# Kernel tuning notes

Hardware: AMD Instinct MI355X
Metric: run time of the kernel (lower is better)

The kernel has to match this reference:

```python
import jax, jax.numpy as jnp
import numpy as np

N, E = 50000, 800000
VOCAB, D, H, EDIM = 10000, 128, 8, 16
C = D // H  # per-head channels = 16
NEG_SLOPE_ATT = 0.2   # GATv2 attention leaky_relu slope
NEG_SLOPE_OUT = 0.01  # F.leaky_relu default
BN_EPS = 1e-5


def setup_inputs() -> dict:
    key = jax.random.key(0)
    ks = jax.random.split(key, 10)
    g = lambda k, shape, fan: (jax.random.normal(k, shape, jnp.float32) / np.float32(np.sqrt(fan)))
    return {
        "x": jax.random.randint(ks[0], (N,), 0, VOCAB),
        "ei": jax.random.randint(ks[1], (2, E), 0, N),
        "ew": jax.random.normal(ks[2], (E, EDIM), jnp.float32),
        "emb": g(ks[3], (VOCAB, D), D),
        "W_l": g(ks[4], (D, D), D),
        "b_l": jnp.zeros((D,), jnp.float32),
        "W_r": g(ks[5], (D, D), D),
        "b_r": jnp.zeros((D,), jnp.float32),
        "att": g(ks[6], (H, C), C),
        "W_e": g(ks[7], (EDIM, D), EDIM),
        "bias": jnp.zeros((D,), jnp.float32),
        "gamma": jnp.ones((D,), jnp.float32),
        "beta": jnp.zeros((D,), jnp.float32),
    }


def reference(x, ei, ew, emb, W_l, b_l, W_r, b_r, att, W_e, bias, gamma, beta):
    n = x.shape[0]
    # Embeddings: lut(x) * sqrt(d_model); dropout=0 (identity)
    h = emb[x] * jnp.float32(np.sqrt(D))                      # [N, D]
    # GATv2Conv linear transforms (source / target)
    xl = (h @ W_l + b_l).reshape(n, H, C)                      # [N, H, C]
    xr = (h @ W_r + b_r).reshape(n, H, C)                      # [N, H, C]
    eemb = (ew @ W_e).reshape(-1, H, C)                        # [E, H, C]
    src, dst = ei[0], ei[1]
    # per-edge attention logits: a^T LeakyReLU(x_l[j] + x_r[i] + e)
    m = jax.nn.leaky_relu(xl[src] + xr[dst] + eemb, NEG_SLOPE_ATT)  # [E, H, C]
    score = jnp.einsum('ehc,hc->eh', m, att)                   # [E, H]
    # segment softmax over incoming edges of each target node
    smax = jax.ops.segment_max(score, dst, num_segments=n)     # [N, H]
    ex = jnp.exp(score - smax[dst])                            # [E, H]
    denom = jax.ops.segment_sum(ex, dst, num_segments=n)       # [N, H]
    alpha = ex / denom[dst]                                    # [E, H]
    # scatter-add aggregation of weighted source features
    agg = jax.ops.segment_sum(alpha[:, :, None] * xl[src], dst, num_segments=n)
    out = agg.reshape(n, D) + bias                             # [N, D]
    # BatchNorm1d (training mode: batch statistics, biased variance)
    mean = out.mean(axis=0)
    var = out.var(axis=0)
    y = (out - mean) * jax.lax.rsqrt(var + BN_EPS) * gamma + beta
    return jax.nn.leaky_relu(y, NEG_SLOPE_OUT)
```

## Files before the change

kernel.cpp:

```cpp
#include <hip/hip_runtime.h>
#include <hip/hip_bf16.h>
#include <hip/hip_fp16.h>

typedef __hip_bfloat16 bf16;
typedef unsigned short u16;

#define D 128
#define EDIM 16
#define SQRT_D 11.313708498984761f

typedef short bf16x8 __attribute__((ext_vector_type(8)));
typedef float f32x4 __attribute__((ext_vector_type(4)));
typedef _Float16 h2 __attribute__((ext_vector_type(2)));

#define PF_BL    0
#define PF_BR    128
#define PF_WE    256
#define PF_ATT   2304
#define PF_BIAS  2432
#define PF_GAMMA 2560
#define PF_BETA  2688
#define PF_TOTAL 2816

__device__ __forceinline__ u16 f2bf_bits(float f) {
    union { bf16 h; u16 s; } cv; cv.h = __float2bfloat16(f); return cv.s;
}
__device__ __forceinline__ float2 h2f2(unsigned u) {
    union { unsigned u; __half2 h; } cv; cv.u = u;
    return __half22float2(cv.h);
}
__device__ __forceinline__ int swid(int nn, int k) {
    return nn * 128 + ((((k >> 3) ^ (nn & 15)) << 3) | (k & 7));
}
__device__ __forceinline__ float red8(float x) {
    x += __int_as_float(__builtin_amdgcn_update_dpp(0, __float_as_int(x), 0xB1, 0xf, 0xf, true));
    x += __int_as_float(__builtin_amdgcn_update_dpp(0, __float_as_int(x), 0x4E, 0xf, 0xf, true));
    x += __int_as_float(__builtin_amdgcn_update_dpp(0, __float_as_int(x), 0x141, 0xf, 0xf, true));
    return x;
}

__global__ void k_zero_detect(int* p, int count, const u16* __restrict__ u, int* flag)
{
    int i = blockIdx.x * blockDim.x + threadIdx.x;
    if (i < count) p[i] = 0;
    if (blockIdx.x == 0) {
        __shared__ int sh[256];
        int t = threadIdx.x;
        int cnt = 0;
        for (int k = t; k < 4096; k += 256) {
            int e = (u[k] >> 7) & 0xFF;
            cnt += (e > 132 && e < 255) ? 1 : 0;
        }
        sh[t] = cnt;
        __syncthreads();
        for (int s = 128; s > 0; s >>= 1) {
            if (t < s) sh[t] += sh[t + s];
            __syncthreads();
        }
        if (t == 0) *flag = (sh[0] > 100) ? 1 : 0;
    }
}

__device__ __forceinline__ float rdv(const void* p, int i, int fl) {
    return fl ? ((const float*)p)[i] : __bfloat162float(((const bf16*)p)[i]);
}

__global__ __launch_bounds__(256) void k_prep_hist(
    const void* Wl, const void* Wr,
    const void* bl, const void* br, const void* We, const void* att,
    const void* bias, const void* gamma, const void* beta,
    const int* __restrict__ flag,
    u16* __restrict__ WT, float* __restrict__ pf,
    const int* __restrict__ ei, int* __restrict__ deg,
    int nE, int prepBlocks)
{
    if ((int)blockIdx.x >= prepBlocks) {
        int e = (blockIdx.x - prepBlocks) * 256 + threadIdx.x;
        if (e < nE) atomicAdd(&deg[ei[nE + e]], 1);
        return;
    }
    const int fl = *flag;
    int idx = blockIdx.x * 256 + threadIdx.x;
    if (idx < 32768) {
        int w = idx >> 14;
        int j = idx & 16383;
        int k = j >> 7, nn = j & 127;
        const void* W = w ? Wr : Wl;
        WT[w * 16384 + swid(nn, k)] = f2bf_bits(rdv(W, k * D + nn, fl) * SQRT_D);
        return;
    }
    idx -= 32768;
    if (idx < 128)  { pf[PF_BL + idx] = rdv(bl, idx, fl); return; }
    idx -= 128;
    if (idx < 128)  { pf[PF_BR + idx] = rdv(br, idx, fl); return; }
    idx -= 128;
    if (idx < 2048) { pf[PF_WE + idx] = rdv(We, idx, fl); return; }
    idx -= 2048;
    if (idx < 128)  { pf[PF_ATT + idx] = rdv(att, idx, fl); return; }
    idx -= 128;
    if (idx < 128)  { pf[PF_BIAS + idx] = rdv(bias, idx, fl); return; }
    idx -= 128;
    if (idx < 128)  { pf[PF_GAMMA + idx] = rdv(gamma, idx, fl); return; }
    idx -= 128;
    if (idx < 128)  { pf[PF_BETA + idx] = rdv(beta, idx, fl); return; }
}

__global__ __launch_bounds__(1024) void k_scan1(
    const int* __restrict__ deg, int* __restrict__ row_ptr,
    int* __restrict__ cursor, int n, int nBlk)
{
    __shared__ int chsum[512];
    __shared__ int part[1024];
    __shared__ int myOff;
    const int t = threadIdx.x;
    const int wv = t >> 6;
    const int lane = t & 63;

    for (int c = wv; c < nBlk; c += 16) {
        int base = c << 10;
        int s = 0;
        for (int k = lane; k < 1024; k += 64) {
            int i = base + k;
            s += (i < n) ? deg[i] : 0;
        }
        #pragma unroll
        for (int m = 1; m < 64; m <<= 1) s += __shfl_xor(s, m);
        if (lane == 0) chsum[c] = s;
    }
    __syncthreads();
    if (t == 0) {
        int run = 0;
        for (int c = 0; c < (int)blockIdx.x; ++c) run += chsum[c];
        myOff = run;
    }
    __syncthreads();

    int i = blockIdx.x * 1024 + t;
    int v = (i < n) ? deg[i] : 0;
    part[t] = v;
    __syncthreads();
    for (int off = 1; off < 1024; off <<= 1) {
        int u = (t >= off) ? part[t - off] : 0;
        __syncthreads();
        part[t] += u;
        __syncthreads();
    }
    if (i < n) {
        int excl = myOff + part[t] - v;
        row_ptr[i] = excl;
        cursor[i] = excl;
        if (i == n - 1) row_ptr[n] = excl + v;
    }
}

__global__ __launch_bounds__(1024) void k_scan_sum(
    const int* __restrict__ deg, int* __restrict__ blkSum, int n)
{
    __shared__ int sh[1024];
    int t = threadIdx.x;
    int i = blockIdx.x * 1024 + t;
    sh[t] = (i < n) ? deg[i] : 0;
    __syncthreads();
    for (int s = 512; s > 0; s >>= 1) {
        if (t < s) sh[t] += sh[t + s];
        __syncthreads();
    }
    if (t == 0) blkSum[blockIdx.x] = sh[0];
}
__global__ __launch_bounds__(1024) void k_scan_blk(
    const int* __restrict__ blkSum, int* __restrict__ blkOff, int nBlk)
{
    __shared__ int part[1024];
    int t = threadIdx.x;
    int v = (t < nBlk) ? blkSum[t] : 0;
    part[t] = v;
    __syncthreads();
    for (int off = 1; off < 1024; off <<= 1) {
        int u = (t >= off) ? part[t - off] : 0;
        __syncthreads();
        part[t] += u;
        __syncthreads();
    }
    if (t < nBlk) blkOff[t] = part[t] - v;
}
__global__ __launch_bounds__(1024) void k_scan_write(
    const int* __restrict__ deg, const int* __restrict__ blkOff,
    int* __restrict__ row_ptr, int* __restrict__ cursor, int n)
{
    __shared__ int part[1024];
    int t = threadIdx.x;
    int i = blockIdx.x * 1024 + t;
    int v = (i < n) ? deg[i] : 0;
    part[t] = v;
    __syncthreads();
    for (int off = 1; off < 1024; off <<= 1) {
        int u = (t >= off) ? part[t - off] : 0;
        __syncthreads();
        part[t] += u;
        __syncthreads();
    }
    if (i < n) {
        int excl = blkOff[blockIdx.x] + part[t] - v;
        row_ptr[i] = excl;
        cursor[i] = excl;
        if (i == n - 1) row_ptr[n] = excl + v;
    }
}

__global__ __launch_bounds__(512) void k_scatnode(
    const int* __restrict__ ei, int* __restrict__ cursor,
    int* __restrict__ csr, const void* __restrict__ ew,
    u16* __restrict__ ewc, const int* __restrict__ flag, int nE,
    const int* __restrict__ x, const void* __restrict__ emb,
    const u16* __restrict__ WT, const float* __restrict__ pf,
    u16* __restrict__ xl16, u16* __restrict__ xr16, int n, int scatBlocks)
{
    __shared__ u16 Bt[16384];
    const int t = threadIdx.x;

    if ((int)blockIdx.x < scatBlocks) {
        int e = blockIdx.x * 512 + t;
        if (e >= nE) return;
        int src = ei[e], dst = ei[nE + e];
        int pos = atomicAdd(&cursor[dst], 1);
        csr[pos] = src << 8;
        __half2 h[8];
        if (*flag) {
            const float4* s = (const float4*)((const float*)ew + (size_t)e * 16);
            float f[16];
            *(float4*)(f)      = s[0];
            *(float4*)(f + 4)  = s[1];
            *(float4*)(f + 8)  = s[2];
            *(float4*)(f + 12) = s[3];
            #pragma unroll
            for (int q = 0; q < 8; ++q)
                h[q] = __float22half2_rn(make_float2(f[2*q], f[2*q+1]));
        } else {
            const uint4* s = (const uint4*)((const u16*)ew + (size_t)e * 16);
            unsigned uu[8];
            *(uint4*)(uu)     = s[0];
            *(uint4*)(uu + 4) = s[1];
            #pragma unroll
            for (int q = 0; q < 8; ++q) {
                float lo = __uint_as_float(uu[q] << 16);
                float hi = __uint_as_float(uu[q] & 0xffff0000u);
                h[q] = __float22half2_rn(make_float2(lo, hi));
            }
        }
        u16* d16 = ewc + ((size_t)pos << 4);
        *(uint4*)d16       = *(uint4*)&h[0];
        *(uint4*)(d16 + 8) = *(uint4*)&h[4];
        return;
    }

    const int fl = *flag;
    const int l = t & 63;
    const int wv = t >> 6;
    const int m = l & 15;
    const int quad = l >> 4;
    const int R = (blockIdx.x - scatBlocks) * 128;

    int arow = R + wv * 16 + m;
    int tok = (arow < n) ? x[arow] : 0;
    bf16x8 afr[4];
    if (!fl) {
        const u16* ap = (const u16*)emb + (size_t)tok * D + quad * 8;
        #pragma unroll
        for (int kk = 0; kk < 4; ++kk) afr[kk] = *(const bf16x8*)(ap + kk * 32);
    } else {
        const float* ap = (const float*)emb + (size_t)tok * D + quad * 8;
        #pragma unroll
        for (int kk = 0; kk < 4; ++kk) {
            float4 a = *(const float4*)(ap + kk * 32);
            float4 b = *(const float4*)(ap + kk * 32 + 4);
            u16 o[8] = { f2bf_bits(a.x), f2bf_bits(a.y), f2bf_bits(a.z), f2bf_bits(a.w),
                         f2bf_bits(b.x), f2bf_bits(b.y), f2bf_bits(b.z), f2bf_bits(b.w) };
            afr[kk] = *(bf16x8*)o;
        }
    }

    #pragma unroll
    for (int w = 0; w < 2; ++w) {
        {
            const uint4* s = (const uint4*)(WT + w * 16384);
            uint4* dd = (uint4*)&Bt[0];
            #pragma unroll
            for (int i = 0; i < 4; ++i) dd[i * 512 + t] = s[i * 512 + t];
        }
        __syncthreads();
        const float* bb = pf + (w ? PF_BR : PF_BL);
        u16* out = w ? xr16 : xl16;
        f32x4 acc[8];
        #pragma unroll
        for (int nt = 0; nt < 8; ++nt) {
            float bv = bb[nt * 16 + m];
            acc[nt] = f32x4{bv, bv, bv, bv};
        }
        #pragma unroll
        for (int kk = 0; kk < 4; ++kk) {
            #pragma unroll
            for (int nt = 0; nt < 8; ++nt) {
                int blk = (quad + 4 * kk) ^ m;
                bf16x8 bfr = *(const bf16x8*)&Bt[(nt * 16 + m) * 128 + blk * 8];
                acc[nt] = __builtin_amdgcn_mfma_f32_16x16x32_bf16(afr[kk], bfr, acc[nt], 0, 0, 0);
            }
        }
        #pragma unroll
        for (int nt = 0; nt < 8; ++nt) {
            int col = nt * 16 + m;
            #pragma unroll
            for (int r = 0; r < 4; ++r) {
                int row = R + wv * 16 + quad * 4 + r;
                if (row < n)
                    out[(size_t)row * D + col] =
                        __half_as_ushort(__float2half(acc[nt][r]));
            }
        }
        __syncthreads();
    }
}

struct EwH {
    unsigned v[8];
    __device__ __forceinline__ void load(const u16* base, int j) {
        const uint4* q = (const uint4*)(base + ((size_t)j << 4));
        uint4 A = q[0], B = q[1];
        v[0]=A.x; v[1]=A.y; v[2]=A.z; v[3]=A.w;
        v[4]=B.x; v[5]=B.y; v[6]=B.z; v[7]=B.w;
    }
    __device__ __forceinline__ float2 pair(int q) const { return h2f2(v[q]); }
};

__global__ __launch_bounds__(256) void k_agg(
    const int* __restrict__ row_ptr, const int* __restrict__ csr,
    const u16* __restrict__ ewc, const float* __restrict__ pf,
    const u16* __restrict__ xl16, const u16* __restrict__ xr16,
    float* __restrict__ vpre, float* __restrict__ bnsum,
    float* __restrict__ bnsumsq, int n)
{
    const int t = threadIdx.x;
    const int l = t & 63;
    const int wv = __builtin_amdgcn_readfirstlane(t >> 6);

#if __has_builtin(__builtin_amdgcn_fdot2)
    h2 we0[8], we1[8];
    #pragma unroll
    for (int q = 0; q < 8; ++q) {
        float2 a = *(const float2*)&pf[PF_WE + (2*q)   * D + 2 * l];
        float2 b = *(const float2*)&pf[PF_WE + (2*q+1) * D + 2 * l];
        we0[q] = h2{(_Float16)a.x, (_Float16)b.x};
        we1[q] = h2{(_Float16)a.y, (_Float16)b.y};
    }
#else
    float2 we[EDIM];
    #pragma unroll
    for (int k = 0; k < EDIM; ++k)
        we[k] = *(const float2*)&pf[PF_WE + k * D + 2 * l];
#endif
    const float2 attv  = *(const float2*)&pf[PF_ATT + 2 * l];
    const float2 biasv = *(const float2*)&pf[PF_BIAS + 2 * l];

    float s0 = 0, s20 = 0, s1 = 0, s21 = 0;

    const int slot = blockIdx.x * 4 + wv;
    const int i0 = slot * 4;
    const int i1 = min(i0 + 4, n);

    if (i0 < n) {
        const char* xlB = (const char*)xl16 + 4 * l;
        const char* xrB = (const char*)xr16 + 4 * l;

        int cur = i0;
        int endCur  = row_ptr[i0 + 1];
        int endNext = row_ptr[min(i0 + 2, i1)];
        const int begAll = row_ptr[i0];
        const int endAll = row_ptr[i1];

        float2 xrvCur  = h2f2(*(const unsigned*)(xrB + ((size_t)i0 << 8)));
        int nxt0 = min(i0 + 1, i1 - 1);
        float2 xrvNext = h2f2(*(const unsigned*)(xrB + ((size_t)nxt0 << 8)));

        float acc0 = 0, acc1 = 0, den = 0;

        auto finalize = [&]() {
            float inv = den > 0.f ? 1.0f / den : 0.0f;
            float v0 = fmaf(acc0, inv, biasv.x);
            float v1 = fmaf(acc1, inv, biasv.y);
            *(float2*)(vpre + ((size_t)cur << 7) + 2 * l) = make_float2(v0, v1);
            s0 += v0; s20 += v0 * v0;
            s1 += v1; s21 += v1 * v1;
            acc0 = acc1 = den = 0.f;
        };
        auto advance = [&]() {
            finalize();
            ++cur;
            endCur  = endNext;
            endNext = row_ptr[min(cur + 2, i1)];
            xrvCur  = xrvNext;
            int nxt = min(cur + 1, i1 - 1);
            xrvNext = h2f2(*(const unsigned*)(xrB + ((size_t)nxt << 8)));
        };
        auto comp = [&](const EwH& w, unsigned xbits) {
            float e0 = xrvCur.x, e1 = xrvCur.y;
#if __has_builtin(__builtin_amdgcn_fdot2)
            #pragma unroll
            for (int q = 0; q < 8; ++q) {
                h2 pr = __builtin_bit_cast(h2, w.v[q]);
                e0 = __builtin_amdgcn_fdot2(pr, we0[q], e0, false);
                e1 = __builtin_amdgcn_fdot2(pr, we1[q], e1, false);
            }
#else
            #pragma unroll
            for (int q = 0; q < 8; ++q) {
                float2 pr = w.pair(q);
                e0 = fmaf(pr.x, we[2*q].x,   e0);
                e0 = fmaf(pr.y, we[2*q+1].x, e0);
                e1 = fmaf(pr.x, we[2*q].y,   e1);
                e1 = fmaf(pr.y, we[2*q+1].y, e1);
            }
#endif
            float2 xc = h2f2(xbits);
            float z0 = xc.x + e0, z1 = xc.y + e1;
            float m0 = fmaxf(z0, 0.2f * z0);
            float m1 = fmaxf(z1, 0.2f * z1);
            float p = red8(fmaf(m1, attv.y, m0 * attv.x));
            float ex = __expf(p);
            den += ex;
            acc0 = fmaf(ex, xc.x, acc0);
            acc1 = fmaf(ex, xc.y, acc1);
        };

        const int cnt = endAll - begAll;
        if (cnt > 0) {
            EwH wA, wB, wC, wD;
            unsigned xA = 0, xB = 0, xC = 0, xD = 0;
            {            wA.load(ewc, begAll);     xA = *(const unsigned*)(xlB + csr[begAll]); }
            if (cnt > 1) { wB.load(ewc, begAll + 1); xB = *(const unsigned*)(xlB + csr[begAll + 1]); }
            if (cnt > 2) { wC.load(ewc, begAll + 2); xC = *(const unsigned*)(xlB + csr[begAll + 2]); }
            if (cnt > 3) { wD.load(ewc, begAll + 3); xD = *(const unsigned*)(xlB + csr[begAll + 3]); }

            int j  = begAll;
            int jp = begAll + 4;
            while (true) {
#define STAGE(W, X)                                                              \
                while (j >= endCur) advance();                                   \
                comp(W, X);                                                      \
                if (jp < endAll) {                                               \
                    W.load(ewc, jp);                                             \
                    X = *(const unsigned*)(xlB + csr[jp]);                       \
                }                                                                \
                ++jp; ++j;                                                       \
                if (j >= endAll) break;
                STAGE(wA, xA)
                STAGE(wB, xB)
                STAGE(wC, xC)
                STAGE(wD, xD)
#undef STAGE
            }
        }
        while (cur < i1) { finalize(); ++cur; }
    }

    __shared__ float sh[4][D], sh2[4][D];
    sh[wv][2*l] = s0;   sh[wv][2*l+1] = s1;
    sh2[wv][2*l] = s20; sh2[wv][2*l+1] = s21;
    __syncthreads();
    if (t < D) {
        float a = 0, a2 = 0;
        #pragma unroll
        for (int q = 0; q < 4; ++q) { a += sh[q][t]; a2 += sh2[q][t]; }
        atomicAdd(&bnsum[t], a);
        atomicAdd(&bnsumsq[t], a2);
    }
}

__global__ __launch_bounds__(256) void k_final(
    const float* __restrict__ vpre, const float* __restrict__ pf,
    const float* __restrict__ bnsum, const float* __restrict__ bnsumsq,
    float* __restrict__ out, int n)
{
    int idx = blockIdx.x * 256 + threadIdx.x;
    if (idx >= n * (D / 4)) return;
    int pos = idx * 4;
    int d = pos & (D - 1);
    const float invN = 1.0f / (float)n;
    float4 v  = *(const float4*)(vpre + pos);
    float4 ms = *(const float4*)(bnsum + d);
    float4 m2 = *(const float4*)(bnsumsq + d);
    float4 g  = *(const float4*)(pf + PF_GAMMA + d);
    float4 bt = *(const float4*)(pf + PF_BETA + d);
    float* vv = (float*)&v; float* msv = (float*)&ms; float* m2v = (float*)&m2;
    float* gv = (float*)&g; float* btv = (float*)&bt;
    float4 o;
    float* ov = (float*)&o;
    #pragma unroll
    for (int c = 0; c < 4; ++c) {
        float mean = msv[c] * invN;
        float var = m2v[c] * invN - mean * mean;
        float y = (vv[c] - mean) * rsqrtf(var + 1e-5f) * gv[c] + btv[c];
        ov[c] = y > 0.f ? y : 0.01f * y;
    }
    *(float4*)(out + pos) = o;
}

extern "C" void kernel_launch(void* const* d_in, const int* in_sizes, int n_in,
                              void* d_out, int out_size, void* d_ws, size_t ws_size,
                              hipStream_t stream)
{
    const int*  x     = (const int*)d_in[0];
    const int*  ei    = (const int*)d_in[1];
    const void* ew    = d_in[2];
    const void* emb   = d_in[3];
    const void* Wl    = d_in[4];
    const void* bl    = d_in[5];
    const void* Wr    = d_in[6];
    const void* br    = d_in[7];
    const void* att   = d_in[8];
    const void* We    = d_in[9];
    const void* bias  = d_in[10];
    const void* gamma = d_in[11];
    const void* beta  = d_in[12];

    const int n  = in_sizes[0];
    const int nE = in_sizes[1] / 2;

    const int nScanBlk = (n + 1023) / 1024;

    float* ws      = (float*)d_ws;
    float* vpre    = ws;
    u16*   xl16    = (u16*)(vpre + (size_t)n * D);
    u16*   xr16    = xl16 + (size_t)n * D;
    int*   deg     = (int*)(xr16 + (size_t)n * D);
    float* bnsum   = (float*)(deg + n);
    float* bnsumsq = bnsum + D;
    int*   flag    = (int*)(bnsumsq + D);
    int*   row_ptr = flag + 1;
    int*   cursor  = row_ptr + (n + 1);
    int*   blkSum  = cursor + n;
    int*   blkOff  = blkSum + nScanBlk;
    uintptr_t p    = (uintptr_t)(blkOff + nScanBlk);
    p = (p + 15) & ~(uintptr_t)15;
    int*   csr     = (int*)p;
    p = (uintptr_t)(csr + nE);
    p = (p + 15) & ~(uintptr_t)15;
    u16*   WT      = (u16*)p;
    p = (uintptr_t)(WT + 32768);
    float* pf      = (float*)p;
    p = (uintptr_t)(pf + PF_TOTAL);
    p = (p + 15) & ~(uintptr_t)15;
    u16*   ewc     = (u16*)p;

    int zc = n + 2 * D;
    k_zero_detect<<<(zc + 255) / 256, 256, 0, stream>>>(deg, zc, (const u16*)emb, flag);

    int prepN = 32768 + PF_TOTAL;
    int prepBlocks = (prepN + 255) / 256;
    int histBlocks = (nE + 255) / 256;
    k_prep_hist<<<prepBlocks + histBlocks, 256, 0, stream>>>(
        Wl, Wr, bl, br, We, att, bias, gamma, beta,
        flag, WT, pf, ei, deg, nE, prepBlocks);

    if (nScanBlk <= 512) {
        k_scan1<<<nScanBlk, 1024, 0, stream>>>(deg, row_ptr, cursor, n, nScanBlk);
    } else {
        k_scan_sum<<<nScanBlk, 1024, 0, stream>>>(deg, blkSum, n);
        k_scan_blk<<<1, 1024, 0, stream>>>(blkSum, blkOff, nScanBlk);
        k_scan_write<<<nScanBlk, 1024, 0, stream>>>(deg, blkOff, row_ptr, cursor, n);
    }

    int scatBlocks = (nE + 511) / 512;
    int nodeBlocks = (n + 127) / 128;
    k_scatnode<<<scatBlocks + nodeBlocks, 512, 0, stream>>>(
        ei, cursor, csr, ew, ewc, flag, nE,
        x, emb, WT, pf, xl16, xr16, n, scatBlocks);

    int aggBlocks = (n + 15) / 16;
    k_agg<<<aggBlocks, 256, 0, stream>>>(row_ptr, csr, ewc, pf, xl16, xr16,
                                         vpre, bnsum, bnsumsq, n);

    k_final<<<(n * (D / 4) + 255) / 256, 256, 0, stream>>>(
        vpre, pf, bnsum, bnsumsq, (float*)d_out, n);
}
```

Before: 348.6 us.

## Shard degree histogram and CSR cursors across 8 copies to reduce atomic contention

Degree counting and CSR scatter cursors are split into 8 per-shard arrays, selected by block index, so edges in different shards hit different atomic addresses. The scan kernels sum the shards to form row pointers and assign each shard its own cursor sub-range within the node's segment. This adds 8x larger zeroing and strided scan reads in exchange for less atomic serialization. Histogram blocks now process two edges per thread so their edge ranges align with the scatter blocks.

```diff
diff --git a/kernel.cpp b/kernel.cpp
--- a/kernel.cpp
+++ b/kernel.cpp
@@ -8,6 +8,7 @@
 #define D 128
 #define EDIM 16
 #define SQRT_D 11.313708498984761f
+#define NSHARD 8
 
 typedef short bf16x8 __attribute__((ext_vector_type(8)));
 typedef float f32x4 __attribute__((ext_vector_type(4)));
@@ -71,12 +72,17 @@
     const void* bias, const void* gamma, const void* beta,
     const int* __restrict__ flag,
     u16* __restrict__ WT, float* __restrict__ pf,
-    const int* __restrict__ ei, int* __restrict__ deg,
-    int nE, int prepBlocks)
+    const int* __restrict__ ei, int* __restrict__ degS,
+    int nE, int nNodes, int prepBlocks)
 {
     if ((int)blockIdx.x >= prepBlocks) {
-        int e = (blockIdx.x - prepBlocks) * 256 + threadIdx.x;
-        if (e < nE) atomicAdd(&deg[ei[nE + e]], 1);
+        int eb = blockIdx.x - prepBlocks;
+        int shard = eb & (NSHARD - 1);
+        int* dS = degS + shard * nNodes;
+        int e0 = eb * 512 + threadIdx.x;
+        if (e0 < nE) atomicAdd(&dS[ei[nE + e0]], 1);
+        int e1 = e0 + 256;
+        if (e1 < nE) atomicAdd(&dS[ei[nE + e1]], 1);
         return;
     }
     const int fl = *flag;
@@ -106,8 +112,8 @@
 }
 
 __global__ __launch_bounds__(1024) void k_scan1(
-    const int* __restrict__ deg, int* __restrict__ row_ptr,
-    int* __restrict__ cursor, int n, int nBlk)
+    const int* __restrict__ degS, int* __restrict__ row_ptr,
+    int* __restrict__ cursorS, int n, int nBlk)
 {
     __shared__ int chsum[512];
     __shared__ int part[1024];
@@ -121,7 +127,10 @@
         int s = 0;
         for (int k = lane; k < 1024; k += 64) {
             int i = base + k;
-            s += (i < n) ? deg[i] : 0;
+            if (i < n) {
+                #pragma unroll
+                for (int sh = 0; sh < NSHARD; ++sh) s += degS[sh * n + i];
+            }
         }
         #pragma unroll
         for (int m = 1; m < 64; m <<= 1) s += __shfl_xor(s, m);
@@ -136,7 +145,12 @@
     __syncthreads();
 
     int i = blockIdx.x * 1024 + t;
-    int v = (i < n) ? deg[i] : 0;
+    int dsh[NSHARD];
+    int v = 0;
+    if (i < n) {
+        #pragma unroll
+        for (int sh = 0; sh < NSHARD; ++sh) { dsh[sh] = degS[sh * n + i]; v += dsh[sh]; }
+    }
     part[t] = v;
     __syncthreads();
     for (int off = 1; off < 1024; off <<= 1) {
@@ -148,18 +162,25 @@
     if (i < n) {
         int excl = myOff + part[t] - v;
         row_ptr[i] = excl;
-        cursor[i] = excl;
+        int run = excl;
+        #pragma unroll
+        for (int sh = 0; sh < NSHARD; ++sh) { cursorS[sh * n + i] = run; run += dsh[sh]; }
         if (i == n - 1) row_ptr[n] = excl + v;
     }
 }
 
 __global__ __launch_bounds__(1024) void k_scan_sum(
-    const int* __restrict__ deg, int* __restrict__ blkSum, int n)
+    const int* __restrict__ degS, int* __restrict__ blkSum, int n)
 {
     __shared__ int sh[1024];
     int t = threadIdx.x;
     int i = blockIdx.x * 1024 + t;
-    sh[t] = (i < n) ? deg[i] : 0;
+    int v = 0;
+    if (i < n) {
+        #pragma unroll
+        for (int s = 0; s < NSHARD; ++s) v += degS[s * n + i];
+    }
+    sh[t] = v;
     __syncthreads();
     for (int s = 512; s > 0; s >>= 1) {
         if (t < s) sh[t] += sh[t + s];
@@ -184,13 +205,18 @@
     if (t < nBlk) blkOff[t] = part[t] - v;
 }
 __global__ __launch_bounds__(1024) void k_scan_write(
-    const int* __restrict__ deg, const int* __restrict__ blkOff,
-    int* __restrict__ row_ptr, int* __restrict__ cursor, int n)
+    const int* __restrict__ degS, const int* __restrict__ blkOff,
+    int* __restrict__ row_ptr, int* __restrict__ cursorS, int n)
 {
     __shared__ int part[1024];
     int t = threadIdx.x;
     int i = blockIdx.x * 1024 + t;
-    int v = (i < n) ? deg[i] : 0;
+    int dsh[NSHARD];
+    int v = 0;
+    if (i < n) {
+        #pragma unroll
+        for (int sh = 0; sh < NSHARD; ++sh) { dsh[sh] = degS[sh * n + i]; v += dsh[sh]; }
+    }
     part[t] = v;
     __syncthreads();
     for (int off = 1; off < 1024; off <<= 1) {
@@ -202,13 +228,15 @@
     if (i < n) {
         int excl = blkOff[blockIdx.x] + part[t] - v;
         row_ptr[i] = excl;
-        cursor[i] = excl;
+        int run = excl;
+        #pragma unroll
+        for (int sh = 0; sh < NSHARD; ++sh) { cursorS[sh * n + i] = run; run += dsh[sh]; }
         if (i == n - 1) row_ptr[n] = excl + v;
     }
 }
 
 __global__ __launch_bounds__(512) void k_scatnode(
-    const int* __restrict__ ei, int* __restrict__ cursor,
+    const int* __restrict__ ei, int* __restrict__ cursorS,
     int* __restrict__ csr, const void* __restrict__ ew,
     u16* __restrict__ ewc, const int* __restrict__ flag, int nE,
     const int* __restrict__ x, const void* __restrict__ emb,
@@ -222,7 +250,8 @@
         int e = blockIdx.x * 512 + t;
         if (e >= nE) return;
         int src = ei[e], dst = ei[nE + e];
-        int pos = atomicAdd(&cursor[dst], 1);
+        int shard = blockIdx.x & (NSHARD - 1);
+        int pos = atomicAdd(&cursorS[shard * n + dst], 1);
         csr[pos] = src << 8;
         __half2 h[8];
         if (*flag) {
@@ -530,13 +559,13 @@
     float* vpre    = ws;
     u16*   xl16    = (u16*)(vpre + (size_t)n * D);
     u16*   xr16    = xl16 + (size_t)n * D;
-    int*   deg     = (int*)(xr16 + (size_t)n * D);
-    float* bnsum   = (float*)(deg + n);
+    int*   degS    = (int*)(xr16 + (size_t)n * D);
+    float* bnsum   = (float*)(degS + (size_t)NSHARD * n);
     float* bnsumsq = bnsum + D;
     int*   flag    = (int*)(bnsumsq + D);
     int*   row_ptr = flag + 1;
-    int*   cursor  = row_ptr + (n + 1);
-    int*   blkSum  = cursor + n;
+    int*   cursorS = row_ptr + (n + 1);
+    int*   blkSum  = cursorS + (size_t)NSHARD * n;
     int*   blkOff  = blkSum + nScanBlk;
     uintptr_t p    = (uintptr_t)(blkOff + nScanBlk);
     p = (p + 15) & ~(uintptr_t)15;
@@ -550,28 +579,28 @@
     p = (p + 15) & ~(uintptr_t)15;
     u16*   ewc     = (u16*)p;
 
-    int zc = n + 2 * D;
-    k_zero_detect<<<(zc + 255) / 256, 256, 0, stream>>>(deg, zc, (const u16*)emb, flag);
+    int zc = NSHARD * n + 2 * D;
+    k_zero_detect<<<(zc + 255) / 256, 256, 0, stream>>>(degS, zc, (const u16*)emb, flag);
 
     int prepN = 32768 + PF_TOTAL;
     int prepBlocks = (prepN + 255) / 256;
-    int histBlocks = (nE + 255) / 256;
+    int histBlocks = (nE + 511) / 512;
     k_prep_hist<<<prepBlocks + histBlocks, 256, 0, stream>>>(
         Wl, Wr, bl, br, We, att, bias, gamma, beta,
-        flag, WT, pf, ei, deg, nE, prepBlocks);
+        flag, WT, pf, ei, degS, nE, n, prepBlocks);
 
     if (nScanBlk <= 512) {
-        k_scan1<<<nScanBlk, 1024, 0, stream>>>(deg, row_ptr, cursor, n, nScanBlk);
+        k_scan1<<<nScanBlk, 1024, 0, stream>>>(degS, row_ptr, cursorS, n, nScanBlk);
     } else {
-        k_scan_sum<<<nScanBlk, 1024, 0, stream>>>(deg, blkSum, n);
+        k_scan_sum<<<nScanBlk, 1024, 0, stream>>>(degS, blkSum, n);
         k_scan_blk<<<1, 1024, 0, stream>>>(blkSum, blkOff, nScanBlk);
-        k_scan_write<<<nScanBlk, 1024, 0, stream>>>(deg, blkOff, row_ptr, cursor, n);
+        k_scan_write<<<nScanBlk, 1024, 0, stream>>>(degS, blkOff, row_ptr, cursorS, n);
     }
 
     int scatBlocks = (nE + 511) / 512;
     int nodeBlocks = (n + 127) / 128;
     k_scatnode<<<scatBlocks + nodeBlocks, 512, 0, stream>>>(
-        ei, cursor, csr, ew, ewc, flag, nE,
+        ei, cursorS, csr, ew, ewc, flag, nE,
         x, emb, WT, pf, xl16, xr16, n, scatBlocks);
 
     int aggBlocks = (n + 15) / 16;
```

Measured after the change: 360.6 us. 3.4% more time.
